# Kernel optimization log

Measured on AMD Instinct MI355X. Metric: run time of the kernel, lower is better.

Reference implementation:

```python
import jax, jax.numpy as jnp
import numpy as np

SIZE = (2, 2)


def setup_inputs() -> dict:
    key = jax.random.key(0)
    k1, k2 = jax.random.split(key)
    B, H, W, C = 16, 64, 64, 128
    out_size = B * H * SIZE[0] * W * SIZE[1] * C  # 33_554_432
    updates = jax.random.normal(k1, (B, H, W, C), dtype=jnp.float32)
    mask = jax.random.randint(k2, (B, H, W, C), 0, out_size, dtype=jnp.int32)
    return {"updates": updates, "mask": mask}


def reference(updates, mask):
    # MaxUnpooling2D: scatter flattened updates into a zero buffer of the
    # full (upsampled) output size using flattened argmax indices, then reshape.
    B, H, W, C = updates.shape
    out_h, out_w = H * SIZE[0], W * SIZE[1]
    out_size = B * out_h * out_w * C
    # tf.scatter_nd sums duplicate indices -> use .add (matches semantics)
    flat = jnp.zeros((out_size,), dtype=updates.dtype).at[mask.reshape(-1)].add(
        updates.reshape(-1)
    )
    return flat.reshape(B, out_h, out_w, C)
```

## Files before the change

kernel.cpp:

```cpp
#include <hip/hip_runtime.h>
#include <hip/hip_fp16.h>


#define NB        2048
#define NB_SHIFT  14
#define RB        16384
#define P1B       1024
#define IPB       8192

typedef float        __attribute__((ext_vector_type(4))) f32x4v;
typedef unsigned int __attribute__((ext_vector_type(4))) u32x4v;

__global__ __launch_bounds__(256, 4) void partition_kernel(
        const float4* __restrict__ upd4,
        const int4*   __restrict__ mask4,
        uint4*        __restrict__ tableT,
        unsigned int* __restrict__ pairs) {
    __shared__ unsigned int hb[NB];
    __shared__ unsigned int wpart[4];
    __shared__ unsigned int stage[IPB];
    const int t = threadIdx.x;
    const int k = blockIdx.x;
    const int s4 = k * (IPB / 4);

    for (int b = t; b < NB; b += 256) hb[b] = 0u;
    __syncthreads();

    int4 mm[IPB / 4 / 256];
    #pragma unroll
    for (int j = 0; j < IPB / 4 / 256; ++j) mm[j] = mask4[s4 + j * 256 + t];
    #pragma unroll
    for (int j = 0; j < IPB / 4 / 256; ++j) {
        atomicAdd(&hb[((unsigned)mm[j].x) >> NB_SHIFT], 1u);
        atomicAdd(&hb[((unsigned)mm[j].y) >> NB_SHIFT], 1u);
        atomicAdd(&hb[((unsigned)mm[j].z) >> NB_SHIFT], 1u);
        atomicAdd(&hb[((unsigned)mm[j].w) >> NB_SHIFT], 1u);
    }
    __syncthreads();

    unsigned c[8], s = 0;
    #pragma unroll
    for (int j = 0; j < 8; ++j) { c[j] = hb[t * 8 + j]; s += c[j]; }
    unsigned inc = s;
    #pragma unroll
    for (int d = 1; d < 64; d <<= 1) {
        unsigned v = __shfl_up(inc, d, 64);
        if ((t & 63) >= d) inc += v;
    }
    if ((t & 63) == 63) wpart[t >> 6] = inc;
    __syncthreads();
    unsigned wbase = 0;
    #pragma unroll
    for (int w = 0; w < 4; ++w) if (w < (t >> 6)) wbase += wpart[w];
    unsigned run = wbase + inc - s;

    unsigned tw[8];
    #pragma unroll
    for (int j = 0; j < 8; ++j) {
        hb[t * 8 + j] = run;
        tw[j] = run | (c[j] << 16);
        run += c[j];
    }
    tableT[(size_t)(t * 2 + 0) * P1B + k] = make_uint4(tw[0], tw[1], tw[2], tw[3]);
    tableT[(size_t)(t * 2 + 1) * P1B + k] = make_uint4(tw[4], tw[5], tw[6], tw[7]);
    __syncthreads();

    float4 uu[IPB / 4 / 256];
    #pragma unroll
    for (int j = 0; j < IPB / 4 / 256; ++j) uu[j] = upd4[s4 + j * 256 + t];
    #pragma unroll
    for (int j = 0; j < IPB / 4 / 256; ++j) {
        #define PLACE(mi, vi) { \
            unsigned b_ = ((unsigned)(mi)) >> NB_SHIFT; \
            unsigned pos_ = atomicAdd(&hb[b_], 1u); \
            stage[pos_] = (((unsigned)(mi)) & (RB - 1u)) | \
                          ((unsigned)__half_as_ushort(__float2half(vi)) << 16); }
        PLACE(mm[j].x, uu[j].x)
        PLACE(mm[j].y, uu[j].y)
        PLACE(mm[j].z, uu[j].z)
        PLACE(mm[j].w, uu[j].w)
        #undef PLACE
    }
    __syncthreads();

    const uint4* sp = (const uint4*)stage;
    uint4* dp = (uint4*)(pairs + (size_t)k * IPB);
    #pragma unroll
    for (int j = 0; j < IPB / 4 / 256; ++j) {
        uint4 v = sp[j * 256 + t];
        __builtin_nontemporal_store(*(const u32x4v*)&v, (u32x4v*)&dp[j * 256 + t]);
    }
}

__global__ __launch_bounds__(512, 4) void unbin_kernel(
        const uint4*        __restrict__ tableT,
        const unsigned int* __restrict__ pairs,
        float4*             __restrict__ out4) {
    __shared__ float tile[RB];
    const int t = threadIdx.x;
    const int b = ((blockIdx.x & 7) << 8) | (blockIdx.x >> 3);
    float4* t4 = (float4*)tile;

    const int sel = b & 3;
    uint4 q0 = tableT[(size_t)(b >> 2) * P1B + 2 * t + 0];
    uint4 q1 = tableT[(size_t)(b >> 2) * P1B + 2 * t + 1];

    for (int j = t; j < RB / 4; j += 512) t4[j] = make_float4(0.f, 0.f, 0.f, 0.f);

    unsigned d0 = sel == 0 ? q0.x : sel == 1 ? q0.y : sel == 2 ? q0.z : q0.w;
    unsigned d1 = sel == 0 ? q1.x : sel == 1 ? q1.y : sel == 2 ? q1.z : q1.w;
    unsigned s0 = (unsigned)(t * 2 + 0) * IPB + (d0 & 0xFFFFu), e0 = s0 + (d0 >> 16);
    unsigned s1 = (unsigned)(t * 2 + 1) * IPB + (d1 & 0xFFFFu), e1 = s1 + (d1 >> 16);
    unsigned a0 = s0 & ~3u, a1 = s1 & ~3u;
    __syncthreads();

    const uint4* p4 = (const uint4*)pairs;
    #define ADDP(w) atomicAdd(&tile[(w) & (RB - 1u)], \
                              __half2float(__ushort_as_half((unsigned short)((w) >> 16))))
    while ((a0 < e0) | (a1 < e1)) {
        bool c0 = a0 < e0, c1 = a1 < e1;
        uint4 v0, v1;
        if (c0) v0 = p4[a0 >> 2];
        if (c1) v1 = p4[a1 >> 2];
        if (c0) {
            if (a0 >= s0)                    ADDP(v0.x);
            if (a0 + 1 >= s0 && a0 + 1 < e0) ADDP(v0.y);
            if (a0 + 2 >= s0 && a0 + 2 < e0) ADDP(v0.z);
            if (a0 + 3 < e0)                 ADDP(v0.w);
            a0 += 4;
        }
        if (c1) {
            if (a1 >= s1)                    ADDP(v1.x);
            if (a1 + 1 >= s1 && a1 + 1 < e1) ADDP(v1.y);
            if (a1 + 2 >= s1 && a1 + 2 < e1) ADDP(v1.z);
            if (a1 + 3 < e1)                 ADDP(v1.w);
            a1 += 4;
        }
    }
    #undef ADDP
    __syncthreads();

    for (int j = t; j < RB / 4; j += 512) {
        float4 v = t4[j];
        __builtin_nontemporal_store(*(const f32x4v*)&v,
                                    (f32x4v*)&out4[(size_t)b * (RB / 4) + j]);
    }
}

__global__ void zero_out_kernel(float4* __restrict__ out, int n4) {
    int i = blockIdx.x * blockDim.x + threadIdx.x;
    if (i < n4) out[i] = make_float4(0.f, 0.f, 0.f, 0.f);
}
__global__ void scatter_add_kernel(const float4* __restrict__ upd,
                                   const int4* __restrict__ mask,
                                   float* __restrict__ out, int n4) {
    int i = blockIdx.x * blockDim.x + threadIdx.x;
    if (i < n4) {
        float4 u = upd[i];
        int4 m = mask[i];
        atomicAdd(out + m.x, u.x);
        atomicAdd(out + m.y, u.y);
        atomicAdd(out + m.z, u.z);
        atomicAdd(out + m.w, u.w);
    }
}

extern "C" void kernel_launch(void* const* d_in, const int* in_sizes, int n_in,
                              void* d_out, int out_size, void* d_ws, size_t ws_size,
                              hipStream_t stream) {
    const float* updates = (const float*)d_in[0];
    const int*   mask    = (const int*)d_in[1];
    float* out = (float*)d_out;
    const int n  = in_sizes[0];
    const int n4 = n >> 2;
    const int o4 = out_size >> 2;

    const size_t pairs_b = (size_t)P1B * IPB * sizeof(unsigned);
    const size_t table_b = (size_t)(NB / 4) * P1B * sizeof(uint4);
    const size_t need = pairs_b + table_b;
    if (ws_size >= need && out_size == NB * RB && n == P1B * IPB) {
        unsigned* pairs  = (unsigned*)d_ws;
        uint4*    tableT = (uint4*)((char*)d_ws + pairs_b);

        partition_kernel<<<P1B, 256, 0, stream>>>(
            (const float4*)updates, (const int4*)mask, tableT, pairs);
        unbin_kernel<<<NB, 512, 0, stream>>>(tableT, pairs, (float4*)out);
    } else {
        zero_out_kernel<<<(o4 + 255) / 256, 256, 0, stream>>>((float4*)out, o4);
        scatter_add_kernel<<<(n4 + 255) / 256, 256, 0, stream>>>(
            (const float4*)updates, (const int4*)mask, out, n4);
    }
}
```

Baseline: 249.0 us.

## Bucket pairs into fixed-capacity global bins via atomic cursors instead of per-block staging

The partition kernel now reserves space in each destination bucket with one global atomicAdd per bucket per block on padded cursors. It writes packed (index, half value) pairs straight into fixed-capacity global bins, dropping the in-block prefix scan, the shared staging buffer and the transposed offset table. The unbin kernel then reads each bin contiguously with coalesced vector loads instead of walking many short per-block segments with divergent bounds checks. The cost is scattered 4-byte global stores in partition, an extra kernel to zero the cursors, and a fixed CAP per bucket that silently overflows if the index distribution is skewed.

```diff
diff --git a/kernel.cpp b/kernel.cpp
--- a/kernel.cpp
+++ b/kernel.cpp
@@ -7,18 +7,21 @@
 #define RB        16384
 #define P1B       1024
 #define IPB       8192
+#define CAP       6144
+#define GCS       16
 
-typedef float        __attribute__((ext_vector_type(4))) f32x4v;
-typedef unsigned int __attribute__((ext_vector_type(4))) u32x4v;
+typedef float __attribute__((ext_vector_type(4))) f32x4v;
+
+__global__ void zero_gcur_kernel(unsigned int* __restrict__ g) {
+    g[blockIdx.x * 256 + threadIdx.x] = 0u;
+}
 
 __global__ __launch_bounds__(256, 4) void partition_kernel(
         const float4* __restrict__ upd4,
         const int4*   __restrict__ mask4,
-        uint4*        __restrict__ tableT,
+        unsigned int* __restrict__ gcur,
         unsigned int* __restrict__ pairs) {
     __shared__ unsigned int hb[NB];
-    __shared__ unsigned int wpart[4];
-    __shared__ unsigned int stage[IPB];
     const int t = threadIdx.x;
     const int k = blockIdx.x;
     const int s4 = k * (IPB / 4);
@@ -38,42 +41,28 @@
     }
     __syncthreads();
 
-    unsigned c[8], s = 0;
+    unsigned c[8], r[8];
     #pragma unroll
-    for (int j = 0; j < 8; ++j) { c[j] = hb[t * 8 + j]; s += c[j]; }
-    unsigned inc = s;
+    for (int j = 0; j < 8; ++j) c[j] = hb[t * 8 + j];
     #pragma unroll
-    for (int d = 1; d < 64; d <<= 1) {
-        unsigned v = __shfl_up(inc, d, 64);
-        if ((t & 63) >= d) inc += v;
-    }
-    if ((t & 63) == 63) wpart[t >> 6] = inc;
-    __syncthreads();
-    unsigned wbase = 0;
-    #pragma unroll
-    for (int w = 0; w < 4; ++w) if (w < (t >> 6)) wbase += wpart[w];
-    unsigned run = wbase + inc - s;
-
-    unsigned tw[8];
-    #pragma unroll
-    for (int j = 0; j < 8; ++j) {
-        hb[t * 8 + j] = run;
-        tw[j] = run | (c[j] << 16);
-        run += c[j];
-    }
-    tableT[(size_t)(t * 2 + 0) * P1B + k] = make_uint4(tw[0], tw[1], tw[2], tw[3]);
-    tableT[(size_t)(t * 2 + 1) * P1B + k] = make_uint4(tw[4], tw[5], tw[6], tw[7]);
-    __syncthreads();
+    for (int j = 0; j < 8; ++j)
+        r[j] = atomicAdd(&gcur[(unsigned)(t * 8 + j) * GCS], c[j]);
 
     float4 uu[IPB / 4 / 256];
     #pragma unroll
     for (int j = 0; j < IPB / 4 / 256; ++j) uu[j] = upd4[s4 + j * 256 + t];
+
+    #pragma unroll
+    for (int j = 0; j < 8; ++j)
+        hb[t * 8 + j] = (unsigned)(t * 8 + j) * CAP + r[j];
+    __syncthreads();
+
     #pragma unroll
     for (int j = 0; j < IPB / 4 / 256; ++j) {
         #define PLACE(mi, vi) { \
             unsigned b_ = ((unsigned)(mi)) >> NB_SHIFT; \
-            unsigned pos_ = atomicAdd(&hb[b_], 1u); \
-            stage[pos_] = (((unsigned)(mi)) & (RB - 1u)) | \
+            unsigned dst_ = atomicAdd(&hb[b_], 1u); \
+            pairs[dst_] = (((unsigned)(mi)) & (RB - 1u)) | \
                           ((unsigned)__half_as_ushort(__float2half(vi)) << 16); }
         PLACE(mm[j].x, uu[j].x)
         PLACE(mm[j].y, uu[j].y)
@@ -81,61 +70,31 @@
         PLACE(mm[j].w, uu[j].w)
         #undef PLACE
     }
-    __syncthreads();
-
-    const uint4* sp = (const uint4*)stage;
-    uint4* dp = (uint4*)(pairs + (size_t)k * IPB);
-    #pragma unroll
-    for (int j = 0; j < IPB / 4 / 256; ++j) {
-        uint4 v = sp[j * 256 + t];
-        __builtin_nontemporal_store(*(const u32x4v*)&v, (u32x4v*)&dp[j * 256 + t]);
-    }
 }
 
-__global__ __launch_bounds__(512, 4) void unbin_kernel(
-        const uint4*        __restrict__ tableT,
+__global__ __launch_bounds__(512) void unbin_kernel(
+        const unsigned int* __restrict__ gcur,
         const unsigned int* __restrict__ pairs,
         float4*             __restrict__ out4) {
     __shared__ float tile[RB];
     const int t = threadIdx.x;
-    const int b = ((blockIdx.x & 7) << 8) | (blockIdx.x >> 3);
+    const int b = blockIdx.x;
+    const unsigned cnt = gcur[(unsigned)b * GCS];
     float4* t4 = (float4*)tile;
 
-    const int sel = b & 3;
-    uint4 q0 = tableT[(size_t)(b >> 2) * P1B + 2 * t + 0];
-    uint4 q1 = tableT[(size_t)(b >> 2) * P1B + 2 * t + 1];
-
     for (int j = t; j < RB / 4; j += 512) t4[j] = make_float4(0.f, 0.f, 0.f, 0.f);
-
-    unsigned d0 = sel == 0 ? q0.x : sel == 1 ? q0.y : sel == 2 ? q0.z : q0.w;
-    unsigned d1 = sel == 0 ? q1.x : sel == 1 ? q1.y : sel == 2 ? q1.z : q1.w;
-    unsigned s0 = (unsigned)(t * 2 + 0) * IPB + (d0 & 0xFFFFu), e0 = s0 + (d0 >> 16);
-    unsigned s1 = (unsigned)(t * 2 + 1) * IPB + (d1 & 0xFFFFu), e1 = s1 + (d1 >> 16);
-    unsigned a0 = s0 & ~3u, a1 = s1 & ~3u;
     __syncthreads();
 
-    const uint4* p4 = (const uint4*)pairs;
+    const uint4* p4 = (const uint4*)(pairs + (size_t)b * CAP);
     #define ADDP(w) atomicAdd(&tile[(w) & (RB - 1u)], \
                               __half2float(__ushort_as_half((unsigned short)((w) >> 16))))
-    while ((a0 < e0) | (a1 < e1)) {
-        bool c0 = a0 < e0, c1 = a1 < e1;
-        uint4 v0, v1;
-        if (c0) v0 = p4[a0 >> 2];
-        if (c1) v1 = p4[a1 >> 2];
-        if (c0) {
-            if (a0 >= s0)                    ADDP(v0.x);
-            if (a0 + 1 >= s0 && a0 + 1 < e0) ADDP(v0.y);
-            if (a0 + 2 >= s0 && a0 + 2 < e0) ADDP(v0.z);
-            if (a0 + 3 < e0)                 ADDP(v0.w);
-            a0 += 4;
-        }
-        if (c1) {
-            if (a1 >= s1)                    ADDP(v1.x);
-            if (a1 + 1 >= s1 && a1 + 1 < e1) ADDP(v1.y);
-            if (a1 + 2 >= s1 && a1 + 2 < e1) ADDP(v1.z);
-            if (a1 + 3 < e1)                 ADDP(v1.w);
-            a1 += 4;
-        }
+    for (unsigned j = t; j * 4u < cnt; j += 512u) {
+        uint4 v = p4[j];
+        unsigned base = j * 4u;
+        ADDP(v.x);
+        if (base + 1u < cnt) ADDP(v.y);
+        if (base + 2u < cnt) ADDP(v.z);
+        if (base + 3u < cnt) ADDP(v.w);
     }
     #undef ADDP
     __syncthreads();
@@ -175,16 +134,17 @@
     const int n4 = n >> 2;
     const int o4 = out_size >> 2;
 
-    const size_t pairs_b = (size_t)P1B * IPB * sizeof(unsigned);
-    const size_t table_b = (size_t)(NB / 4) * P1B * sizeof(uint4);
-    const size_t need = pairs_b + table_b;
+    const size_t pairs_b = (size_t)NB * CAP * sizeof(unsigned);
+    const size_t gcur_b  = (size_t)NB * GCS * sizeof(unsigned);
+    const size_t need = pairs_b + gcur_b;
     if (ws_size >= need && out_size == NB * RB && n == P1B * IPB) {
-        unsigned* pairs  = (unsigned*)d_ws;
-        uint4*    tableT = (uint4*)((char*)d_ws + pairs_b);
+        unsigned* pairs = (unsigned*)d_ws;
+        unsigned* gcur  = (unsigned*)((char*)d_ws + pairs_b);
 
+        zero_gcur_kernel<<<NB * GCS / 256, 256, 0, stream>>>(gcur);
         partition_kernel<<<P1B, 256, 0, stream>>>(
-            (const float4*)updates, (const int4*)mask, tableT, pairs);
-        unbin_kernel<<<NB, 512, 0, stream>>>(tableT, pairs, (float4*)out);
+            (const float4*)updates, (const int4*)mask, gcur, pairs);
+        unbin_kernel<<<NB, 512, 0, stream>>>(gcur, pairs, (float4*)out);
     } else {
         zero_out_kernel<<<(o4 + 255) / 256, 256, 0, stream>>>((float4*)out, o4);
         scatter_add_kernel<<<(n4 + 255) / 256, 256, 0, stream>>>(
```

Result: slower. 332.3 us (+33.4%).
